# Optimization experiments

Hardware: AMD Instinct MI355X
Metric: run time of the kernel (lower is better)

The kernel has to match this reference:

```python
import jax, jax.numpy as jnp
import numpy as np

ANGLE = 0.5  # angular margin from init_kwargs


def setup_inputs() -> dict:
    key = jax.random.key(0)
    k1, k2, k3 = jax.random.split(key, 3)
    B, F, C = 512, 128, 100000
    # scale by 0.1 so exp(features @ w) and exp(modulus * cos) stay finite in fp32
    features = jax.random.normal(k1, (B, F), dtype=jnp.float32) * 0.1
    w = jax.random.normal(k2, (F, C), dtype=jnp.float32) * 0.1
    target = jax.random.randint(k3, (B,), 0, C, dtype=jnp.int64)
    return {"features": features, "w": w, "target": target}


def reference(features, w, target):
    B = features.shape[0]
    rows = jnp.arange(B)
    # norms: [B,1] and [1,C]
    features_modulus = jnp.sqrt(jnp.sum(features ** 2, axis=1, keepdims=True))
    w_modulus = jnp.sqrt(jnp.sum(w ** 2, axis=0, keepdims=True))
    modulus = features_modulus * w_modulus  # [B, C]
    logits = jnp.matmul(features, w)  # [B, C] (computed once; torch computes it twice)
    cos_theta = logits / modulus / 1.01
    theta = jnp.arccos(cos_theta) + ANGLE
    cos_theta_plus = jnp.cos(theta)
    margin_logits = modulus * cos_theta_plus  # [B, C]
    top = jnp.exp(margin_logits[rows, target])  # [B]
    down_ = jnp.exp(logits)  # [B, C]
    down = jnp.sum(down_, axis=1) - down_[rows, target] + top  # [B]
    return -jnp.sum(jnp.log(top / down)) / B
```

## Files before the change

kernel.cpp:

```cpp
#include <hip/hip_runtime.h>

#define F_DIM 128
#define C_DIM 100000
#define B_ROWS 512
#define ANGLE 0.5f
#define CPB 128
#define NCB 782
#define OOB_PAD 96.0f
#define LBT_S 136

typedef __attribute__((ext_vector_type(4))) float  f32x4;
typedef __attribute__((ext_vector_type(8))) short  bf16x8;
typedef __attribute__((ext_vector_type(4))) short  bf16x4;

static __device__ __forceinline__ short f2bf(float x) {
    unsigned int u = __float_as_uint(x);
    u += 0x7FFFu + ((u >> 16) & 1u);
    return (short)(u >> 16);
}

__global__ __launch_bounds__(1024, 4)
void arc_main(const float* __restrict__ feat,
              const float* __restrict__ w,
              float* __restrict__ pp)
{
    __shared__ unsigned short lBt[128 * LBT_S];

    const int tid = threadIdx.x;
    const int cb  = blockIdx.x;
    const int c0  = cb * CPB;

    {
        const int c  = tid & 127;
        const int g  = tid >> 7;
        const int gc = c0 + c;
        float v[16];
        #pragma unroll
        for (int i = 0; i < 16; ++i)
            v[i] = (gc < C_DIM) ? w[(size_t)(g * 16 + i) * C_DIM + gc] : 0.f;
        #pragma unroll
        for (int j = 0; j < 4; ++j) {
            bf16x4 h;
            h[0] = f2bf(v[4*j+0]); h[1] = f2bf(v[4*j+1]);
            h[2] = f2bf(v[4*j+2]); h[3] = f2bf(v[4*j+3]);
            *(bf16x4*)&lBt[c * LBT_S + g * 16 + j * 4] = h;
        }
    }

    const int lane = tid & 63;
    const int wv   = tid >> 6;
    const int quad = lane >> 4;
    const int l15  = lane & 15;

    bf16x8 fB[2][4];
    #pragma unroll
    for (int s = 0; s < 2; ++s) {
        const int b = wv * 32 + s * 16 + l15;
        #pragma unroll
        for (int ks = 0; ks < 4; ++ks) {
            const int k0 = ks * 32 + quad * 8;
            const f32x4 u0 = *(const f32x4*)(feat + b * F_DIM + k0);
            const f32x4 u1 = *(const f32x4*)(feat + b * F_DIM + k0 + 4);
            bf16x8 h;
            h[0] = f2bf(u0[0]); h[1] = f2bf(u0[1]); h[2] = f2bf(u0[2]); h[3] = f2bf(u0[3]);
            h[4] = f2bf(u1[0]); h[5] = f2bf(u1[1]); h[6] = f2bf(u1[2]); h[7] = f2bf(u1[3]);
            fB[s][ks] = h;
        }
    }
    __syncthreads();

    float esum0 = 0.f, esum1 = 0.f;
    #pragma unroll
    for (int m = 0; m < 8; ++m) {
        f32x4 a0 = {0.f, 0.f, 0.f, 0.f};
        f32x4 a1 = {0.f, 0.f, 0.f, 0.f};
        #pragma unroll
        for (int ks = 0; ks < 4; ++ks) {
            const bf16x8 af =
                *(const bf16x8*)&lBt[(m * 16 + l15) * LBT_S + ks * 32 + quad * 8];
            a0 = __builtin_amdgcn_mfma_f32_16x16x32_bf16(af, fB[0][ks], a0, 0, 0, 0);
            a1 = __builtin_amdgcn_mfma_f32_16x16x32_bf16(af, fB[1][ks], a1, 0, 0, 0);
        }
        #pragma unroll
        for (int r = 0; r < 4; ++r) {
            esum0 += __expf(a0[r]);
            esum1 += __expf(a1[r]);
        }
    }

    esum0 += __shfl_xor(esum0, 16); esum0 += __shfl_xor(esum0, 32);
    esum1 += __shfl_xor(esum1, 16); esum1 += __shfl_xor(esum1, 32);
    if (lane < 16) {
        pp[(size_t)cb * 512 + wv * 32 + lane]      = esum0;
        pp[(size_t)cb * 512 + wv * 32 + 16 + lane] = esum1;
    }
}

__global__ void arc_row(const float* __restrict__ feat,
                        const float* __restrict__ w,
                        const int*   __restrict__ target,
                        const float* __restrict__ pp,
                        float* __restrict__ term)
{
    const int b    = blockIdx.x;
    const int lane = threadIdx.x;
    const int t    = target[b];

    float dot = 0.f, wsq = 0.f, fsq = 0.f, rs = 0.f;
    #pragma unroll
    for (int h = 0; h < 2; ++h) {
        const int f  = lane + h * 64;
        const float fv = feat[b * F_DIM + f];
        const float wv = w[(size_t)f * C_DIM + t];
        dot += fv * wv;
        wsq += wv * wv;
        fsq += fv * fv;
    }
    for (int j = lane; j < NCB; j += 64)
        rs += pp[(size_t)j * 512 + b];

    #pragma unroll
    for (int off = 32; off > 0; off >>= 1) {
        dot += __shfl_xor(dot, off);
        wsq += __shfl_xor(wsq, off);
        fsq += __shfl_xor(fsq, off);
        rs  += __shfl_xor(rs,  off);
    }
    if (lane == 0) {
        const float mod = sqrtf(fsq) * sqrtf(wsq);
        float ct = dot / (mod * 1.01f);
        ct = fminf(1.f, fmaxf(-1.f, ct));
        const float th   = acosf(ct) + ANGLE;
        const float marg = mod * cosf(th);
        const float down = rs - OOB_PAD - expf(dot) + expf(marg);
        term[b] = marg - logf(down);
    }
}

__global__ void arc_loss(const float* __restrict__ term,
                         float* __restrict__ out)
{
    __shared__ float red[B_ROWS];
    const int b = threadIdx.x;
    red[b] = term[b];
    __syncthreads();
    #pragma unroll
    for (int st = 256; st > 0; st >>= 1) {
        if (b < st) red[b] += red[b + st];
        __syncthreads();
    }
    if (b == 0) out[0] = -red[0] / (float)B_ROWS;
}

extern "C" void kernel_launch(void* const* d_in, const int* in_sizes, int n_in,
                              void* d_out, int out_size, void* d_ws, size_t ws_size,
                              hipStream_t stream)
{
    const float* feat   = (const float*)d_in[0];
    const float* w      = (const float*)d_in[1];
    const int*   target = (const int*)d_in[2];

    float* pp   = (float*)d_ws;
    float* term = pp + (size_t)NCB * 512;

    arc_main<<<NCB, 1024, 0, stream>>>(feat, w, pp);
    arc_row<<<B_ROWS, 64, 0, stream>>>(feat, w, target, pp, term);
    arc_loss<<<1, B_ROWS, 0, stream>>>(term, (float*)d_out);
}
```

Measured before the change: 135.8 us.

## Split batch rows across two blocks, swizzle LDS layout, widen bf16 stores

The main kernel now launches a 2D grid in which each 512-thread block covers half of the 512 batch rows for a 128-column tile. The padded LDS tile is replaced by an unpadded layout with an XOR swizzle, written with 8-wide bf16 stores to avoid bank conflicts. The feature fragment loads are moved ahead of the weight staging, and the exp accumulation is split into independent partial sums to shorten dependency chains. In exchange, each weight tile is loaded and converted twice (once per row half), doubling weight traffic and conversion work while giving more, smaller blocks for occupancy.

```diff
diff --git a/kernel.cpp b/kernel.cpp
--- a/kernel.cpp
+++ b/kernel.cpp
@@ -7,11 +7,9 @@
 #define CPB 128
 #define NCB 782
 #define OOB_PAD 96.0f
-#define LBT_S 136
 
 typedef __attribute__((ext_vector_type(4))) float  f32x4;
 typedef __attribute__((ext_vector_type(8))) short  bf16x8;
-typedef __attribute__((ext_vector_type(4))) short  bf16x4;
 
 static __device__ __forceinline__ short f2bf(float x) {
     unsigned int u = __float_as_uint(x);
@@ -19,33 +17,17 @@
     return (short)(u >> 16);
 }
 
-__global__ __launch_bounds__(1024, 4)
+__global__ __launch_bounds__(512, 4)
 void arc_main(const float* __restrict__ feat,
               const float* __restrict__ w,
               float* __restrict__ pp)
 {
-    __shared__ unsigned short lBt[128 * LBT_S];
+    __shared__ unsigned short lBt[128 * 128];
 
     const int tid = threadIdx.x;
     const int cb  = blockIdx.x;
     const int c0  = cb * CPB;
-
-    {
-        const int c  = tid & 127;
-        const int g  = tid >> 7;
-        const int gc = c0 + c;
-        float v[16];
-        #pragma unroll
-        for (int i = 0; i < 16; ++i)
-            v[i] = (gc < C_DIM) ? w[(size_t)(g * 16 + i) * C_DIM + gc] : 0.f;
-        #pragma unroll
-        for (int j = 0; j < 4; ++j) {
-            bf16x4 h;
-            h[0] = f2bf(v[4*j+0]); h[1] = f2bf(v[4*j+1]);
-            h[2] = f2bf(v[4*j+2]); h[3] = f2bf(v[4*j+3]);
-            *(bf16x4*)&lBt[c * LBT_S + g * 16 + j * 4] = h;
-        }
-    }
+    const int r0  = blockIdx.y * 256;
 
     const int lane = tid & 63;
     const int wv   = tid >> 6;
@@ -55,7 +37,7 @@
     bf16x8 fB[2][4];
     #pragma unroll
     for (int s = 0; s < 2; ++s) {
-        const int b = wv * 32 + s * 16 + l15;
+        const int b = r0 + wv * 32 + s * 16 + l15;
         #pragma unroll
         for (int ks = 0; ks < 4; ++ks) {
             const int k0 = ks * 32 + quad * 8;
@@ -67,32 +49,55 @@
             fB[s][ks] = h;
         }
     }
+
+    {
+        const int c  = tid & 127;
+        const int g  = tid >> 7;
+        const int gc = c0 + c;
+        #pragma unroll
+        for (int j = 0; j < 4; ++j) {
+            float v[8];
+            #pragma unroll
+            for (int i = 0; i < 8; ++i) {
+                const int k = g * 32 + j * 8 + i;
+                v[i] = (gc < C_DIM) ? w[(size_t)k * C_DIM + gc] : 0.f;
+            }
+            bf16x8 h;
+            #pragma unroll
+            for (int i = 0; i < 8; ++i) h[i] = f2bf(v[i]);
+            const int pc = (g * 4 + j) ^ (c & 15);
+            *(bf16x8*)&lBt[c * 128 + pc * 8] = h;
+        }
+    }
     __syncthreads();
 
-    float esum0 = 0.f, esum1 = 0.f;
+    float eA0 = 0.f, eA1 = 0.f, eA2 = 0.f, eA3 = 0.f;
+    float eB0 = 0.f, eB1 = 0.f, eB2 = 0.f, eB3 = 0.f;
     #pragma unroll
     for (int m = 0; m < 8; ++m) {
         f32x4 a0 = {0.f, 0.f, 0.f, 0.f};
         f32x4 a1 = {0.f, 0.f, 0.f, 0.f};
+        const int row = m * 16 + l15;
         #pragma unroll
         for (int ks = 0; ks < 4; ++ks) {
-            const bf16x8 af =
-                *(const bf16x8*)&lBt[(m * 16 + l15) * LBT_S + ks * 32 + quad * 8];
+            const int pc = (ks * 4 + quad) ^ (row & 15);
+            const bf16x8 af = *(const bf16x8*)&lBt[row * 128 + pc * 8];
             a0 = __builtin_amdgcn_mfma_f32_16x16x32_bf16(af, fB[0][ks], a0, 0, 0, 0);
             a1 = __builtin_amdgcn_mfma_f32_16x16x32_bf16(af, fB[1][ks], a1, 0, 0, 0);
         }
-        #pragma unroll
-        for (int r = 0; r < 4; ++r) {
-            esum0 += __expf(a0[r]);
-            esum1 += __expf(a1[r]);
-        }
+        eA0 += __expf(a0[0]); eA1 += __expf(a0[1]);
+        eA2 += __expf(a0[2]); eA3 += __expf(a0[3]);
+        eB0 += __expf(a1[0]); eB1 += __expf(a1[1]);
+        eB2 += __expf(a1[2]); eB3 += __expf(a1[3]);
     }
 
+    float esum0 = (eA0 + eA1) + (eA2 + eA3);
+    float esum1 = (eB0 + eB1) + (eB2 + eB3);
     esum0 += __shfl_xor(esum0, 16); esum0 += __shfl_xor(esum0, 32);
     esum1 += __shfl_xor(esum1, 16); esum1 += __shfl_xor(esum1, 32);
     if (lane < 16) {
-        pp[(size_t)cb * 512 + wv * 32 + lane]      = esum0;
-        pp[(size_t)cb * 512 + wv * 32 + 16 + lane] = esum1;
+        pp[(size_t)cb * 512 + r0 + wv * 32 + lane]      = esum0;
+        pp[(size_t)cb * 512 + r0 + wv * 32 + 16 + lane] = esum1;
     }
 }
 
@@ -163,7 +168,7 @@
     float* pp   = (float*)d_ws;
     float* term = pp + (size_t)NCB * 512;
 
-    arc_main<<<NCB, 1024, 0, stream>>>(feat, w, pp);
+    arc_main<<<dim3(NCB, 2), 512, 0, stream>>>(feat, w, pp);
     arc_row<<<B_ROWS, 64, 0, stream>>>(feat, w, target, pp, term);
     arc_loss<<<1, B_ROWS, 0, stream>>>(term, (float*)d_out);
 }
```

Result: faster. 131.4 us (-3.2%).
